# Kernel tuning notes

Measured on AMD Instinct MI355X. Metric: run time of the kernel, lower is better.

The kernel has to match this reference:

```python
import jax, jax.numpy as jnp
import numpy as np

MAXG = 8          # max adaptive sampling grid (boxes generated so ceil(roi_size) <= 8)
SCALE = 0.125     # spatial_scale / ds (ds = 1.0)


def setup_inputs() -> dict:
    key = jax.random.key(0)
    ks = jax.random.split(key, 12)
    bs, N, ch, H, W = 8, 128, 1280, 64, 64
    out_ch, inner = 1024, 5120
    z = jax.random.normal(ks[0], (bs, ch, H, W), jnp.float32)
    # boxes (x1, y1, x2, y2) in 512x512 image coords, sizes in [8, 64] px
    x1 = jax.random.uniform(ks[1], (bs, N), minval=0.0, maxval=448.0)
    y1 = jax.random.uniform(ks[2], (bs, N), minval=0.0, maxval=448.0)
    bw = jax.random.uniform(ks[3], (bs, N), minval=8.0, maxval=64.0)
    bh = jax.random.uniform(ks[4], (bs, N), minval=8.0, maxval=64.0)
    bboxes = jnp.stack([x1, y1, x1 + bw, y1 + bh], axis=-1)

    def lin(k, fan_in, shape):
        return jax.random.normal(k, shape, jnp.float32) * (1.0 / np.sqrt(fan_in))

    W1 = lin(ks[5], ch, (ch, inner)); b1 = jnp.zeros((inner,), jnp.float32)
    W2 = lin(ks[6], inner, (inner, out_ch)); b2 = jnp.zeros((out_ch,), jnp.float32)
    S1 = lin(ks[7], 2, (2, 64)); sb1 = jnp.zeros((64,), jnp.float32)
    S2 = lin(ks[8], 64, (64, 256)); sb2 = jnp.zeros((256,), jnp.float32)
    S3 = lin(ks[9], 256, (256, out_ch)); sb3 = jnp.zeros((out_ch,), jnp.float32)
    O = lin(ks[10], 2 * out_ch, (2 * out_ch, out_ch)); ob = jnp.zeros((out_ch,), jnp.float32)
    return dict(z=z, bboxes=bboxes, W1=W1, b1=b1, W2=W2, b2=b2,
                S1=S1, sb1=sb1, S2=S2, sb2=sb2, S3=S3, sb3=sb3, O=O, ob=ob)


def _prep(c, size):
    # torchvision bilinear border handling for one coordinate axis
    oob = (c < -1.0) | (c > size)
    cc = jnp.clip(c, 0.0, None)
    lo0 = jnp.floor(cc)
    hi_case = lo0 >= size - 1
    lo = jnp.minimum(lo0, size - 1).astype(jnp.int32)
    hi = jnp.minimum(lo0 + 1, size - 1).astype(jnp.int32)
    frac = jnp.where(hi_case, 0.0, cc - lo0)
    return lo, hi, frac, oob


def _roi_align_1x1(z, bboxes):
    # torchvision roi_align, output_size=1, aligned=True, sampling_ratio=-1
    bs, ch, H, W = z.shape
    N = bboxes.shape[1]
    boxes = jax.lax.stop_gradient(bboxes).reshape(-1, 4) * SCALE - 0.5  # aligned
    bidx = jnp.repeat(jnp.arange(bs), N)
    rw = boxes[:, 2] - boxes[:, 0]
    rh = boxes[:, 3] - boxes[:, 1]
    gw = jnp.clip(jnp.ceil(rw), 1, MAXG)   # adaptive grid: ceil(roi_size / 1)
    gh = jnp.clip(jnp.ceil(rh), 1, MAXG)
    count = gh * gw
    i = jnp.arange(MAXG, dtype=jnp.float32)
    ys = boxes[:, 1:2] + (i[None] + 0.5) * rh[:, None] / gh[:, None]  # [R, G]
    xs = boxes[:, 0:1] + (i[None] + 0.5) * rw[:, None] / gw[:, None]
    vy = i[None] < gh[:, None]
    vx = i[None] < gw[:, None]
    yl, yh, fy, oy = _prep(ys, H)
    xl, xh, fx, ox = _prep(xs, W)
    my = (vy & ~oy).astype(z.dtype)
    mx = (vx & ~ox).astype(z.dtype)
    mask = my[:, :, None] * mx[:, None, :]             # [R, G, G]
    hy, ly = 1.0 - fy, fy
    hx, lx = 1.0 - fx, fx
    zt = jnp.transpose(z, (0, 2, 3, 1))                # [bs, H, W, ch]
    acc = jnp.zeros((bs * N, ch), z.dtype)
    corners = [(yl, xl, hy, hx), (yl, xh, hy, lx), (yh, xl, ly, hx), (yh, xh, ly, lx)]
    for yi, xi, wy, wx in corners:
        wt = mask * (wy[:, :, None] * wx[:, None, :])  # [R, G, G]
        v = zt[bidx[:, None, None], yi[:, :, None], xi[:, None, :]]  # [R, G, G, ch]
        acc = acc + jnp.einsum('rgh,rghc->rc', wt, v)
    return (acc / count[:, None]).reshape(bs, N, ch)


def reference(z, bboxes, W1, b1, W2, b2, S1, sb1, S2, sb2, S3, sb3, O, ob):
    x = _roi_align_1x1(z, bboxes)                      # [bs, N, ch]
    x = jax.nn.relu(x @ W1 + b1) @ W2 + b2             # out MLP
    # BBoxSizeEmbedder: (h, w) = (y2 - y1, x2 - x1)
    sz = jnp.stack([bboxes[..., 3] - bboxes[..., 1],
                    bboxes[..., 2] - bboxes[..., 0]], axis=-1)
    e = jax.nn.relu(sz @ S1 + sb1)
    e = jax.nn.relu(e @ S2 + sb2)
    e = e @ S3 + sb3
    return jnp.concatenate([x, e], axis=-1) @ O + ob   # out2
```

## Files before the change

kernel.cpp:

```cpp
#include <hip/hip_runtime.h>

static constexpr int kBS    = 8;
static constexpr int kNROI  = 128;
static constexpr int kR     = kBS * kNROI;
static constexpr int kCH    = 1280;
static constexpr int kH     = 64;
static constexpr int kW     = 64;
static constexpr int kPIX   = kH * kW;
static constexpr int kINNER = 5120;
static constexpr int kOUTC  = 1024;
static constexpr int kXE    = 2 * kOUTC;
static constexpr int kE2    = 256;

typedef _Float16 half8 __attribute__((ext_vector_type(8)));
typedef float floatx4 __attribute__((ext_vector_type(4)));

__device__ __forceinline__ void gload_lds16(const _Float16* g, _Float16* l) {
    __builtin_amdgcn_global_load_lds(
        (const __attribute__((address_space(1))) void*)g,
        (__attribute__((address_space(3))) void*)l,
        16, 0, 0);
}

static constexpr int kPrepConvEnd = 13824;
static constexpr int kPrepMlpEnd  = 14080;
static constexpr int kPrepAllEnd  = 14080 + (kPIX / 64) * (kCH / 64) * kBS;

__global__ __launch_bounds__(256) void prep_all(const float* __restrict__ z,
                                                _Float16* __restrict__ zt,
                                                const float* __restrict__ W1,
                                                const float* __restrict__ W2,
                                                const float* __restrict__ O,
                                                const float* __restrict__ S3,
                                                _Float16* __restrict__ W1t,
                                                _Float16* __restrict__ W2t,
                                                _Float16* __restrict__ Ot,
                                                _Float16* __restrict__ S3t,
                                                const float* __restrict__ bboxes,
                                                const float* __restrict__ S1,
                                                const float* __restrict__ sb1,
                                                const float* __restrict__ S2,
                                                const float* __restrict__ sb2,
                                                _Float16* __restrict__ h2f) {
    __shared__ float smem[64 * 65];
    const int bid = blockIdx.x;
    const int t   = threadIdx.x;

    if (bid < kPrepConvEnd) {
        const float* W; _Float16* Wt; int K, N, tile;
        if (bid < 6400)        { W = W1; Wt = W1t; K = kCH;    N = kINNER; tile = bid; }
        else if (bid < 11520)  { W = W2; Wt = W2t; K = kINNER; N = kOUTC;  tile = bid - 6400; }
        else if (bid < 13568)  { W = O;  Wt = Ot;  K = kXE;    N = kOUTC;  tile = bid - 11520; }
        else                   { W = S3; Wt = S3t; K = kE2;    N = kOUTC;  tile = bid - 13568; }
        const int nt = N / 32;
        const int n0 = (tile % nt) * 32;
        const int k0 = (tile / nt) * 32;
        {
            const int row = t >> 3;
            const int c4  = (t & 7) * 4;
            const float4 v = *(const float4*)&W[(size_t)(k0 + row) * N + n0 + c4];
            float* tl = smem + row * 33 + c4;
            tl[0] = v.x; tl[1] = v.y; tl[2] = v.z; tl[3] = v.w;
        }
        __syncthreads();
        {
            const int n  = t >> 3;
            const int k4 = (t & 7) * 4;
            union { _Float16 h[4]; uint2 u; } pk;
#pragma unroll
            for (int j = 0; j < 4; ++j) pk.h[j] = (_Float16)smem[(k4 + j) * 33 + n];
            *(uint2*)&Wt[(size_t)(n0 + n) * K + k0 + k4] = pk.u;
        }
    } else if (bid < kPrepMlpEnd) {
        const int r0 = (bid - kPrepConvEnd) * 4;
        float* sz = smem;
        float* h1 = smem + 8;
        if (t < 8) {
            const int row = t >> 1;
            const int c   = t & 1;
            const float* bb = bboxes + (size_t)(r0 + row) * 4;
            sz[row * 2 + c] = (c == 0) ? (bb[3] - bb[1]) : (bb[2] - bb[0]);
        }
        __syncthreads();
        {
            const int row = t >> 6;
            const int j   = t & 63;
            const float v = sz[row * 2] * S1[j] + sz[row * 2 + 1] * S1[64 + j] + sb1[j];
            h1[row * 64 + j] = fmaxf(v, 0.0f);
        }
        __syncthreads();
        {
            float acc[4];
            const float b = sb2[t];
#pragma unroll
            for (int row = 0; row < 4; ++row) acc[row] = b;
#pragma unroll 16
            for (int k = 0; k < 64; ++k) {
                const float w = S2[k * 256 + t];
#pragma unroll
                for (int row = 0; row < 4; ++row) acc[row] += h1[row * 64 + k] * w;
            }
#pragma unroll
            for (int row = 0; row < 4; ++row)
                h2f[(size_t)(r0 + row) * kE2 + t] = (_Float16)fmaxf(acc[row], 0.0f);
        }
    } else {
        const int tb   = bid - kPrepMlpEnd;
        const int perB = (kPIX / 64) * (kCH / 64);
        const int b    = tb / perB;
        const int rem  = tb - b * perB;
        const int p0 = (rem % (kPIX / 64)) * 64;
        const int c0 = (rem / (kPIX / 64)) * 64;
        const float* zb = z + (size_t)b * kCH * kPIX;
        _Float16* ztb = zt + (size_t)b * kPIX * kCH;
#pragma unroll
        for (int i = 0; i < 4; ++i) {
            const int idx = t + i * 256;
            const int row = idx >> 4;
            const int c4  = (idx & 15) * 4;
            const float4 v = *(const float4*)&zb[(size_t)(c0 + row) * kPIX + p0 + c4];
            float* tl = smem + row * 65 + c4;
            tl[0] = v.x; tl[1] = v.y; tl[2] = v.z; tl[3] = v.w;
        }
        __syncthreads();
#pragma unroll
        for (int i = 0; i < 4; ++i) {
            const int p  = (t >> 4) + i * 16;
            const int c4 = (t & 15) * 4;
            union { _Float16 h[4]; uint2 u; } pk;
#pragma unroll
            for (int j = 0; j < 4; ++j) pk.h[j] = (_Float16)smem[(c4 + j) * 65 + p];
            *(uint2*)(ztb + (size_t)(p0 + p) * kCH + c0 + c4) = pk.u;
        }
    }
}

struct RoiW {
    int   ymin, xmin, nyd, nxd;
    float ywt[12], xwt[12];
    float invCount;
};

__device__ inline void build_wcons(const float* __restrict__ bboxes, int r, RoiW* L) {
    const float x1 = bboxes[r * 4 + 0] * 0.125f - 0.5f;
    const float y1 = bboxes[r * 4 + 1] * 0.125f - 0.5f;
    const float x2 = bboxes[r * 4 + 2] * 0.125f - 0.5f;
    const float y2 = bboxes[r * 4 + 3] * 0.125f - 0.5f;
    const float rw = x2 - x1, rh = y2 - y1;
    const float gwf = fminf(fmaxf(ceilf(rw), 1.0f), 8.0f);
    const float ghf = fminf(fmaxf(ceilf(rh), 1.0f), 8.0f);
    const int gw = (int)gwf, gh = (int)ghf;
    L->invCount = 1.0f / (gwf * ghf);

#pragma unroll
    for (int i = 0; i < 12; ++i) { L->ywt[i] = 0.0f; L->xwt[i] = 0.0f; }

    int ymin = 0, last = 0;
    for (int g = 0; g < gh; ++g) {
        const float c   = y1 + ((float)g + 0.5f) * rh / ghf;
        const bool oob  = (c < -1.0f) || (c > 64.0f);
        const float cc  = fmaxf(c, 0.0f);
        const float lo0 = floorf(cc);
        const bool hic  = (lo0 >= 63.0f);
        const int lo    = (int)fminf(lo0, 63.0f);
        const int hi    = (int)fminf(lo0 + 1.0f, 63.0f);
        const float fr  = hic ? 0.0f : (cc - lo0);
        const float m   = oob ? 0.0f : 1.0f;
        if (g == 0) ymin = lo;
        const int il = min(lo - ymin, 11);
        const int ih = min(hi - ymin, 11);
        L->ywt[il] += m * (1.0f - fr);
        L->ywt[ih] += m * fr;
        last = hi;
    }
    L->ymin = ymin;
    L->nyd  = min(last - ymin + 1, 12);

    int xmin = 0; last = 0;
    for (int g = 0; g < gw; ++g) {
        const float c   = x1 + ((float)g + 0.5f) * rw / gwf;
        const bool oob  = (c < -1.0f) || (c > 64.0f);
        const float cc  = fmaxf(c, 0.0f);
        const float lo0 = floorf(cc);
        const bool hic  = (lo0 >= 63.0f);
        const int lo    = (int)fminf(lo0, 63.0f);
        const int hi    = (int)fminf(lo0 + 1.0f, 63.0f);
        const float fr  = hic ? 0.0f : (cc - lo0);
        const float m   = oob ? 0.0f : 1.0f;
        if (g == 0) xmin = lo;
        const int il = min(lo - xmin, 11);
        const int ih = min(hi - xmin, 11);
        L->xwt[il] += m * (1.0f - fr);
        L->xwt[ih] += m * fr;
        last = hi;
    }
    L->xmin = xmin;
    L->nxd  = min(last - xmin + 1, 12);
}

__global__ __launch_bounds__(256) void roi_gather_f16_v3(const _Float16* __restrict__ zt,
                                                         const float* __restrict__ bboxes,
                                                         _Float16* __restrict__ x) {
    const int r  = blockIdx.y;
    const int b  = r >> 7;
    const int cg = blockIdx.x * 32;
    const int t  = threadIdx.x;
    __shared__ RoiW L;
    __shared__ int   off[144];
    __shared__ float wt[144];
    __shared__ float accs[8][32][9];
    if (t == 0) build_wcons(bboxes, r, &L);
    __syncthreads();
    const int np = L.nyd * L.nxd;
    if (t < np) {
        const int iy = t / L.nxd;
        const int ix = t - iy * L.nxd;
        off[t] = ((L.ymin + iy) * kW + (L.xmin + ix)) * kCH;
        wt[t]  = L.ywt[iy] * L.xwt[ix];
    }
    __syncthreads();
    const int lc = t & 31;
    const int pg = t >> 5;
    const _Float16* base = zt + (size_t)b * kPIX * kCH + (size_t)(cg + lc) * 8;
    float a[8] = {0.f, 0.f, 0.f, 0.f, 0.f, 0.f, 0.f, 0.f};
    for (int p = pg; p < np; p += 8) {
        const float w = wt[p];
        const half8 v = *(const half8*)(base + off[p]);
#pragma unroll
        for (int q = 0; q < 8; ++q) a[q] += w * (float)v[q];
    }
#pragma unroll
    for (int q = 0; q < 8; ++q) accs[pg][lc][q] = a[q];
    __syncthreads();
    const int rc = t >> 3, ch = t & 7;
    float s = 0.f;
#pragma unroll
    for (int g = 0; g < 8; ++g) s += accs[g][rc][ch];
    x[(size_t)r * kCH + (size_t)(cg + rc) * 8 + ch] = (_Float16)(s * L.invCount);
}

__global__ __launch_bounds__(256) void roi_gather_direct(const float* __restrict__ z,
                                                         const float* __restrict__ bboxes,
                                                         _Float16* __restrict__ x) {
    const int r = blockIdx.x;
    const int b = r >> 7;
    __shared__ RoiW L;
    if (threadIdx.x == 0) build_wcons(bboxes, r, &L);
    __syncthreads();
    const float ic = L.invCount;
    const float* zb = z + (size_t)b * kCH * kPIX;
    for (int c = threadIdx.x; c < kCH; c += 256) {
        const float* zc = zb + (size_t)c * kPIX;
        float acc = 0.f;
        for (int iy = 0; iy < L.nyd; ++iy) {
            const float wy = L.ywt[iy];
            const int base = (L.ymin + iy) * kW + L.xmin;
            for (int ix = 0; ix < L.nxd; ++ix)
                acc += wy * L.xwt[ix] * zc[base + ix];
        }
        x[(size_t)r * kCH + c] = (_Float16)(acc * ic);
    }
}

template <int NSPLIT>
__global__ __launch_bounds__(256) void gemm_f16_sk(const _Float16* __restrict__ A,
                                                   const _Float16* __restrict__ Bt,
                                                   float* __restrict__ P,
                                                   int Kfull) {
    __shared__ _Float16 As[2][128 * 32];
    __shared__ _Float16 Bs[2][128 * 32];
    const int t    = threadIdx.x;
    const int lane = t & 63;
    const int wave = t >> 6;
    const int m0 = blockIdx.y * 128, n0 = blockIdx.x * 128;
    const int Ksplit = Kfull / NSPLIT;
    const int s  = blockIdx.z;
    const int Nn = gridDim.x * 128;
    const int Mm = gridDim.y * 128;

    const int c0 = t, c1 = t + 256;
    const _Float16* Ag0 = A + (size_t)(m0 + (c0 >> 2)) * Kfull + (c0 & 3) * 8 + s * Ksplit;
    const _Float16* Ag1 = A + (size_t)(m0 + (c1 >> 2)) * Kfull + (c1 & 3) * 8 + s * Ksplit;
    const _Float16* Bg0 = Bt + (size_t)(n0 + (c0 >> 2)) * Kfull + (c0 & 3) * 8 + s * Ksplit;
    const _Float16* Bg1 = Bt + (size_t)(n0 + (c1 >> 2)) * Kfull + (c1 & 3) * 8 + s * Ksplit;

    const int wm = (wave >> 1) * 64;
    const int wn = (wave & 1) * 64;
    const int fm = lane & 15;
    const int kq = (lane >> 4) * 8;

    floatx4 acc[4][4];
#pragma unroll
    for (int i = 0; i < 4; ++i)
#pragma unroll
        for (int j = 0; j < 4; ++j) acc[i][j] = (floatx4){0.f, 0.f, 0.f, 0.f};

    const int nsteps = Ksplit / 32;
    gload_lds16(Ag0, &As[0][c0 * 8]);
    gload_lds16(Ag1, &As[0][c1 * 8]);
    gload_lds16(Bg0, &Bs[0][c0 * 8]);
    gload_lds16(Bg1, &Bs[0][c1 * 8]);
    __syncthreads();

    for (int ks = 0; ks < nsteps; ++ks) {
        const int cur = ks & 1;
        if (ks + 1 < nsteps) {
            const int kn = (ks + 1) * 32;
            gload_lds16(Ag0 + kn, &As[cur ^ 1][c0 * 8]);
            gload_lds16(Ag1 + kn, &As[cur ^ 1][c1 * 8]);
            gload_lds16(Bg0 + kn, &Bs[cur ^ 1][c0 * 8]);
            gload_lds16(Bg1 + kn, &Bs[cur ^ 1][c1 * 8]);
        }
        half8 af[4], bfv[4];
#pragma unroll
        for (int i = 0; i < 4; ++i)
            af[i] = *(const half8*)&As[cur][(wm + i * 16 + fm) * 32 + kq];
#pragma unroll
        for (int j = 0; j < 4; ++j)
            bfv[j] = *(const half8*)&Bs[cur][(wn + j * 16 + fm) * 32 + kq];
#pragma unroll
        for (int i = 0; i < 4; ++i)
#pragma unroll
            for (int j = 0; j < 4; ++j)
                acc[i][j] = __builtin_amdgcn_mfma_f32_16x16x32_f16(af[i], bfv[j], acc[i][j], 0, 0, 0);
        __syncthreads();
    }

    float* Pp = P + (size_t)s * Mm * Nn;
    const int qr = (lane >> 4) * 4;
#pragma unroll
    for (int j = 0; j < 4; ++j) {
        const int col = n0 + wn + j * 16 + fm;
#pragma unroll
        for (int i = 0; i < 4; ++i) {
            const int row = m0 + wm + i * 16 + qr;
#pragma unroll
            for (int rr = 0; rr < 4; ++rr)
                Pp[(size_t)(row + rr) * Nn + col] = acc[i][j][rr];
        }
    }
}

__global__ __launch_bounds__(256) void gemm_dual(const _Float16* __restrict__ h2f,
                                                 const _Float16* __restrict__ S3t,
                                                 const float* __restrict__ sb3,
                                                 _Float16* __restrict__ xeR,
                                                 const _Float16* __restrict__ x,
                                                 const _Float16* __restrict__ W1t,
                                                 const float* __restrict__ b1,
                                                 _Float16* __restrict__ h) {
    __shared__ _Float16 As[2][128 * 32];
    __shared__ _Float16 Bs[2][128 * 32];
    const int bid = blockIdx.x;
    const _Float16* A; const _Float16* Bt; const float* bias; _Float16* Out;
    int Kfull, ldc, nbn, tile; bool relu;
    if (bid < 64) {
        A = h2f; Bt = S3t; bias = sb3; Out = xeR;
        Kfull = kE2; ldc = kXE; relu = false; nbn = kOUTC / 128; tile = bid;
    } else {
        A = x; Bt = W1t; bias = b1; Out = h;
        Kfull = kCH; ldc = kINNER; relu = true; nbn = kINNER / 128; tile = bid - 64;
    }
    const int n0 = (tile % nbn) * 128;
    const int m0 = (tile / nbn) * 128;

    const int t    = threadIdx.x;
    const int lane = t & 63;
    const int wave = t >> 6;

    const int c0 = t, c1 = t + 256;
    const _Float16* Ag0 = A + (size_t)(m0 + (c0 >> 2)) * Kfull + (c0 & 3) * 8;
    const _Float16* Ag1 = A + (size_t)(m0 + (c1 >> 2)) * Kfull + (c1 & 3) * 8;
    const _Float16* Bg0 = Bt + (size_t)(n0 + (c0 >> 2)) * Kfull + (c0 & 3) * 8;
    const _Float16* Bg1 = Bt + (size_t)(n0 + (c1 >> 2)) * Kfull + (c1 & 3) * 8;

    const int wm = (wave >> 1) * 64;
    const int wn = (wave & 1) * 64;
    const int fm = lane & 15;
    const int kq = (lane >> 4) * 8;

    floatx4 acc[4][4];
#pragma unroll
    for (int i = 0; i < 4; ++i)
#pragma unroll
        for (int j = 0; j < 4; ++j) acc[i][j] = (floatx4){0.f, 0.f, 0.f, 0.f};

    const int nsteps = Kfull / 32;
    gload_lds16(Ag0, &As[0][c0 * 8]);
    gload_lds16(Ag1, &As[0][c1 * 8]);
    gload_lds16(Bg0, &Bs[0][c0 * 8]);
    gload_lds16(Bg1, &Bs[0][c1 * 8]);
    __syncthreads();

    for (int ks = 0; ks < nsteps; ++ks) {
        const int cur = ks & 1;
        if (ks + 1 < nsteps) {
            const int kn = (ks + 1) * 32;
            gload_lds16(Ag0 + kn, &As[cur ^ 1][c0 * 8]);
            gload_lds16(Ag1 + kn, &As[cur ^ 1][c1 * 8]);
            gload_lds16(Bg0 + kn, &Bs[cur ^ 1][c0 * 8]);
            gload_lds16(Bg1 + kn, &Bs[cur ^ 1][c1 * 8]);
        }
        half8 af[4], bfv[4];
#pragma unroll
        for (int i = 0; i < 4; ++i)
            af[i] = *(const half8*)&As[cur][(wm + i * 16 + fm) * 32 + kq];
#pragma unroll
        for (int j = 0; j < 4; ++j)
            bfv[j] = *(const half8*)&Bs[cur][(wn + j * 16 + fm) * 32 + kq];
#pragma unroll
        for (int i = 0; i < 4; ++i)
#pragma unroll
            for (int j = 0; j < 4; ++j)
                acc[i][j] = __builtin_amdgcn_mfma_f32_16x16x32_f16(af[i], bfv[j], acc[i][j], 0, 0, 0);
        __syncthreads();
    }

    const int qr = (lane >> 4) * 4;
#pragma unroll
    for (int j = 0; j < 4; ++j) {
        const int col = n0 + wn + j * 16 + fm;
        const float bv = bias[col];
#pragma unroll
        for (int i = 0; i < 4; ++i) {
            const int row = m0 + wm + i * 16 + qr;
#pragma unroll
            for (int rr = 0; rr < 4; ++rr) {
                float v = acc[i][j][rr] + bv;
                if (relu) v = fmaxf(v, 0.f);
                Out[(size_t)(row + rr) * ldc + col] = (_Float16)v;
            }
        }
    }
}

template <bool RELU, bool F16OUT, int NSPLIT>
__global__ __launch_bounds__(256) void reduce_splitk(const float* __restrict__ P,
                                                     const float* __restrict__ bias,
                                                     void* __restrict__ Cout,
                                                     int Nn, int ldc) {
    const size_t idx = ((size_t)blockIdx.x * 256 + threadIdx.x) * 4;
    const size_t MN  = (size_t)gridDim.x * 1024;
    const int m = (int)(idx / (size_t)Nn);
    const int n = (int)(idx % (size_t)Nn);
    float4 acc = *(const float4*)(P + idx);
#pragma unroll
    for (int s = 1; s < NSPLIT; ++s) {
        const float4 v = *(const float4*)(P + (size_t)s * MN + idx);
        acc.x += v.x; acc.y += v.y; acc.z += v.z; acc.w += v.w;
    }
    const float4 b4 = *(const float4*)(bias + n);
    acc.x += b4.x; acc.y += b4.y; acc.z += b4.z; acc.w += b4.w;
    if (RELU) {
        acc.x = fmaxf(acc.x, 0.f); acc.y = fmaxf(acc.y, 0.f);
        acc.z = fmaxf(acc.z, 0.f); acc.w = fmaxf(acc.w, 0.f);
    }
    if (F16OUT) {
        union { _Float16 h[4]; uint2 u; } pk;
        pk.h[0] = (_Float16)acc.x; pk.h[1] = (_Float16)acc.y;
        pk.h[2] = (_Float16)acc.z; pk.h[3] = (_Float16)acc.w;
        *(uint2*)((_Float16*)Cout + (size_t)m * ldc + n) = pk.u;
    } else {
        *(float4*)((float*)Cout + (size_t)m * ldc + n) = acc;
    }
}

extern "C" void kernel_launch(void* const* d_in, const int* in_sizes, int n_in,
                              void* d_out, int out_size, void* d_ws, size_t ws_size,
                              hipStream_t stream) {
    (void)in_sizes; (void)n_in; (void)out_size;
    const float* z   = (const float*)d_in[0];
    const float* bb  = (const float*)d_in[1];
    const float* W1  = (const float*)d_in[2];
    const float* b1  = (const float*)d_in[3];
    const float* W2  = (const float*)d_in[4];
    const float* b2  = (const float*)d_in[5];
    const float* S1  = (const float*)d_in[6];
    const float* sb1 = (const float*)d_in[7];
    const float* S2  = (const float*)d_in[8];
    const float* sb2 = (const float*)d_in[9];
    const float* S3  = (const float*)d_in[10];
    const float* sb3 = (const float*)d_in[11];
    const float* O   = (const float*)d_in[12];
    const float* ob  = (const float*)d_in[13];
    float* out = (float*)d_out;

    char* ws = (char*)d_ws;
    size_t off = 0;
    auto alloc = [&](size_t bytes) {
        void* p = ws + off;
        off += (bytes + 255) & ~(size_t)255;
        return p;
    };
    _Float16* x    = (_Float16*)alloc((size_t)kR * kCH * 2);
    _Float16* h    = (_Float16*)alloc((size_t)kR * kINNER * 2);
    _Float16* xe   = (_Float16*)alloc((size_t)kR * kXE * 2);
    _Float16* W1t  = (_Float16*)alloc((size_t)kINNER * kCH * 2);
    _Float16* W2t  = (_Float16*)alloc((size_t)kOUTC * kINNER * 2);
    _Float16* Ot   = (_Float16*)alloc((size_t)kOUTC * kXE * 2);
    _Float16* S3t  = (_Float16*)alloc((size_t)kOUTC * kE2 * 2);
    _Float16* h2f  = (_Float16*)alloc((size_t)kR * kE2 * 2);
    float*    P    = (float*)alloc((size_t)8 * kR * kOUTC * 4);
    const size_t ztBytes = (size_t)kBS * kPIX * kCH * 2;
    _Float16* zt  = (_Float16*)(ws + off);
    const bool useT = (off + ztBytes) <= ws_size;

    hipLaunchKernelGGL(prep_all, dim3(useT ? kPrepAllEnd : kPrepMlpEnd), dim3(256), 0,
                       stream, z, zt, W1, W2, O, S3, W1t, W2t, Ot, S3t,
                       bb, S1, sb1, S2, sb2, h2f);

    if (useT) {
        hipLaunchKernelGGL(roi_gather_f16_v3, dim3(kCH / 256, kR), dim3(256), 0, stream,
                           zt, bb, x);
    } else {
        hipLaunchKernelGGL(roi_gather_direct, dim3(kR), dim3(256), 0, stream, z, bb, x);
    }

    hipLaunchKernelGGL(gemm_dual, dim3(64 + (kINNER / 128) * (kR / 128)), dim3(256), 0,
                       stream, h2f, S3t, sb3, xe + kOUTC, x, W1t, b1, h);

    hipLaunchKernelGGL((gemm_f16_sk<8>), dim3(kOUTC / 128, kR / 128, 8), dim3(256), 0,
                       stream, h, W2t, P, kINNER);
    hipLaunchKernelGGL((reduce_splitk<false, true, 8>),
                       dim3((size_t)kR * kOUTC / 1024), dim3(256), 0, stream,
                       P, b2, xe, kOUTC, kXE);

    hipLaunchKernelGGL((gemm_f16_sk<8>), dim3(kOUTC / 128, kR / 128, 8), dim3(256), 0,
                       stream, xe, Ot, P, kXE);
    hipLaunchKernelGGL((reduce_splitk<false, false, 8>),
                       dim3((size_t)kR * kOUTC / 1024), dim3(256), 0, stream,
                       P, ob, out, kOUTC, kOUTC);
}
```

Before: 419.6 us.

## Replace z transpose and ROI gather with per-plane LDS gather using precomputed sample lists

Removes the full fp32-to-fp16 transpose of z into an NHWC buffer. Instead, the prep kernel precomputes each ROI's list of (pixel offset, weight) pairs with the count division folded into the weight. A new gather kernel loads 4 channel planes of z into LDS and walks those lists for all 128 ROIs of an image. This reads z exactly once at fp32 and skips writing and re-reading the transposed copy, at the cost of low per-block parallelism and serial, per-thread list walks that read pixels from LDS.

```diff
diff --git a/kernel.cpp b/kernel.cpp
--- a/kernel.cpp
+++ b/kernel.cpp
@@ -11,6 +11,7 @@
 static constexpr int kOUTC  = 1024;
 static constexpr int kXE    = 2 * kOUTC;
 static constexpr int kE2    = 256;
+static constexpr int kLB    = 144;
 
 typedef _Float16 half8 __attribute__((ext_vector_type(8)));
 typedef float floatx4 __attribute__((ext_vector_type(4)));
@@ -20,119 +21,6 @@
         (const __attribute__((address_space(1))) void*)g,
         (__attribute__((address_space(3))) void*)l,
         16, 0, 0);
-}
-
-static constexpr int kPrepConvEnd = 13824;
-static constexpr int kPrepMlpEnd  = 14080;
-static constexpr int kPrepAllEnd  = 14080 + (kPIX / 64) * (kCH / 64) * kBS;
-
-__global__ __launch_bounds__(256) void prep_all(const float* __restrict__ z,
-                                                _Float16* __restrict__ zt,
-                                                const float* __restrict__ W1,
-                                                const float* __restrict__ W2,
-                                                const float* __restrict__ O,
-                                                const float* __restrict__ S3,
-                                                _Float16* __restrict__ W1t,
-                                                _Float16* __restrict__ W2t,
-                                                _Float16* __restrict__ Ot,
-                                                _Float16* __restrict__ S3t,
-                                                const float* __restrict__ bboxes,
-                                                const float* __restrict__ S1,
-                                                const float* __restrict__ sb1,
-                                                const float* __restrict__ S2,
-                                                const float* __restrict__ sb2,
-                                                _Float16* __restrict__ h2f) {
-    __shared__ float smem[64 * 65];
-    const int bid = blockIdx.x;
-    const int t   = threadIdx.x;
-
-    if (bid < kPrepConvEnd) {
-        const float* W; _Float16* Wt; int K, N, tile;
-        if (bid < 6400)        { W = W1; Wt = W1t; K = kCH;    N = kINNER; tile = bid; }
-        else if (bid < 11520)  { W = W2; Wt = W2t; K = kINNER; N = kOUTC;  tile = bid - 6400; }
-        else if (bid < 13568)  { W = O;  Wt = Ot;  K = kXE;    N = kOUTC;  tile = bid - 11520; }
-        else                   { W = S3; Wt = S3t; K = kE2;    N = kOUTC;  tile = bid - 13568; }
-        const int nt = N / 32;
-        const int n0 = (tile % nt) * 32;
-        const int k0 = (tile / nt) * 32;
-        {
-            const int row = t >> 3;
-            const int c4  = (t & 7) * 4;
-            const float4 v = *(const float4*)&W[(size_t)(k0 + row) * N + n0 + c4];
-            float* tl = smem + row * 33 + c4;
-            tl[0] = v.x; tl[1] = v.y; tl[2] = v.z; tl[3] = v.w;
-        }
-        __syncthreads();
-        {
-            const int n  = t >> 3;
-            const int k4 = (t & 7) * 4;
-            union { _Float16 h[4]; uint2 u; } pk;
-#pragma unroll
-            for (int j = 0; j < 4; ++j) pk.h[j] = (_Float16)smem[(k4 + j) * 33 + n];
-            *(uint2*)&Wt[(size_t)(n0 + n) * K + k0 + k4] = pk.u;
-        }
-    } else if (bid < kPrepMlpEnd) {
-        const int r0 = (bid - kPrepConvEnd) * 4;
-        float* sz = smem;
-        float* h1 = smem + 8;
-        if (t < 8) {
-            const int row = t >> 1;
-            const int c   = t & 1;
-            const float* bb = bboxes + (size_t)(r0 + row) * 4;
-            sz[row * 2 + c] = (c == 0) ? (bb[3] - bb[1]) : (bb[2] - bb[0]);
-        }
-        __syncthreads();
-        {
-            const int row = t >> 6;
-            const int j   = t & 63;
-            const float v = sz[row * 2] * S1[j] + sz[row * 2 + 1] * S1[64 + j] + sb1[j];
-            h1[row * 64 + j] = fmaxf(v, 0.0f);
-        }
-        __syncthreads();
-        {
-            float acc[4];
-            const float b = sb2[t];
-#pragma unroll
-            for (int row = 0; row < 4; ++row) acc[row] = b;
-#pragma unroll 16
-            for (int k = 0; k < 64; ++k) {
-                const float w = S2[k * 256 + t];
-#pragma unroll
-                for (int row = 0; row < 4; ++row) acc[row] += h1[row * 64 + k] * w;
-            }
-#pragma unroll
-            for (int row = 0; row < 4; ++row)
-                h2f[(size_t)(r0 + row) * kE2 + t] = (_Float16)fmaxf(acc[row], 0.0f);
-        }
-    } else {
-        const int tb   = bid - kPrepMlpEnd;
-        const int perB = (kPIX / 64) * (kCH / 64);
-        const int b    = tb / perB;
-        const int rem  = tb - b * perB;
-        const int p0 = (rem % (kPIX / 64)) * 64;
-        const int c0 = (rem / (kPIX / 64)) * 64;
-        const float* zb = z + (size_t)b * kCH * kPIX;
-        _Float16* ztb = zt + (size_t)b * kPIX * kCH;
-#pragma unroll
-        for (int i = 0; i < 4; ++i) {
-            const int idx = t + i * 256;
-            const int row = idx >> 4;
-            const int c4  = (idx & 15) * 4;
-            const float4 v = *(const float4*)&zb[(size_t)(c0 + row) * kPIX + p0 + c4];
-            float* tl = smem + row * 65 + c4;
-            tl[0] = v.x; tl[1] = v.y; tl[2] = v.z; tl[3] = v.w;
-        }
-        __syncthreads();
-#pragma unroll
-        for (int i = 0; i < 4; ++i) {
-            const int p  = (t >> 4) + i * 16;
-            const int c4 = (t & 15) * 4;
-            union { _Float16 h[4]; uint2 u; } pk;
-#pragma unroll
-            for (int j = 0; j < 4; ++j) pk.h[j] = (_Float16)smem[(c4 + j) * 65 + p];
-            *(uint2*)(ztb + (size_t)(p0 + p) * kCH + c0 + c4) = pk.u;
-        }
-    }
 }
 
 struct RoiW {
@@ -198,67 +86,145 @@
     L->nxd  = min(last - xmin + 1, 12);
 }
 
-__global__ __launch_bounds__(256) void roi_gather_f16_v3(const _Float16* __restrict__ zt,
-                                                         const float* __restrict__ bboxes,
+static constexpr int kPrepConvEnd = 13824;
+static constexpr int kPrepMlpEnd  = 14080;
+static constexpr int kPrepAllEnd  = 14084;
+
+__global__ __launch_bounds__(256) void prep_all(const float* __restrict__ W1,
+                                                const float* __restrict__ W2,
+                                                const float* __restrict__ O,
+                                                const float* __restrict__ S3,
+                                                _Float16* __restrict__ W1t,
+                                                _Float16* __restrict__ W2t,
+                                                _Float16* __restrict__ Ot,
+                                                _Float16* __restrict__ S3t,
+                                                const float* __restrict__ bboxes,
+                                                const float* __restrict__ S1,
+                                                const float* __restrict__ sb1,
+                                                const float* __restrict__ S2,
+                                                const float* __restrict__ sb2,
+                                                _Float16* __restrict__ h2f,
+                                                int2* __restrict__ lst,
+                                                int* __restrict__ npA) {
+    __shared__ float smem[32 * 33];
+    const int bid = blockIdx.x;
+    const int t   = threadIdx.x;
+
+    if (bid < kPrepConvEnd) {
+        const float* W; _Float16* Wt; int K, N, tile;
+        if (bid < 6400)        { W = W1; Wt = W1t; K = kCH;    N = kINNER; tile = bid; }
+        else if (bid < 11520)  { W = W2; Wt = W2t; K = kINNER; N = kOUTC;  tile = bid - 6400; }
+        else if (bid < 13568)  { W = O;  Wt = Ot;  K = kXE;    N = kOUTC;  tile = bid - 11520; }
+        else                   { W = S3; Wt = S3t; K = kE2;    N = kOUTC;  tile = bid - 13568; }
+        const int nt = N / 32;
+        const int n0 = (tile % nt) * 32;
+        const int k0 = (tile / nt) * 32;
+        {
+            const int row = t >> 3;
+            const int c4  = (t & 7) * 4;
+            const float4 v = *(const float4*)&W[(size_t)(k0 + row) * N + n0 + c4];
+            float* tl = smem + row * 33 + c4;
+            tl[0] = v.x; tl[1] = v.y; tl[2] = v.z; tl[3] = v.w;
+        }
+        __syncthreads();
+        {
+            const int n  = t >> 3;
+            const int k4 = (t & 7) * 4;
+            union { _Float16 h[4]; uint2 u; } pk;
+#pragma unroll
+            for (int j = 0; j < 4; ++j) pk.h[j] = (_Float16)smem[(k4 + j) * 33 + n];
+            *(uint2*)&Wt[(size_t)(n0 + n) * K + k0 + k4] = pk.u;
+        }
+    } else if (bid < kPrepMlpEnd) {
+        const int r0 = (bid - kPrepConvEnd) * 4;
+        float* sz = smem;
+        float* h1 = smem + 8;
+        if (t < 8) {
+            const int row = t >> 1;
+            const int c   = t & 1;
+            const float* bb = bboxes + (size_t)(r0 + row) * 4;
+            sz[row * 2 + c] = (c == 0) ? (bb[3] - bb[1]) : (bb[2] - bb[0]);
+        }
+        __syncthreads();
+        {
+            const int row = t >> 6;
+            const int j   = t & 63;
+            const float v = sz[row * 2] * S1[j] + sz[row * 2 + 1] * S1[64 + j] + sb1[j];
+            h1[row * 64 + j] = fmaxf(v, 0.0f);
+        }
+        __syncthreads();
+        {
+            float acc[4];
+            const float b = sb2[t];
+#pragma unroll
+            for (int row = 0; row < 4; ++row) acc[row] = b;
+#pragma unroll 16
+            for (int k = 0; k < 64; ++k) {
+                const float w = S2[k * 256 + t];
+#pragma unroll
+                for (int row = 0; row < 4; ++row) acc[row] += h1[row * 64 + k] * w;
+            }
+#pragma unroll
+            for (int row = 0; row < 4; ++row)
+                h2f[(size_t)(r0 + row) * kE2 + t] = (_Float16)fmaxf(acc[row], 0.0f);
+        }
+    } else {
+        const int r = (bid - kPrepMlpEnd) * 256 + t;
+        RoiW L;
+        build_wcons(bboxes, r, &L);
+        int2* lr = lst + (size_t)r * kLB;
+        int p = 0;
+        for (int iy = 0; iy < L.nyd; ++iy) {
+            const float wy = L.ywt[iy] * L.invCount;
+            const int yb   = (L.ymin + iy) * kW + L.xmin;
+            for (int ix = 0; ix < L.nxd; ++ix) {
+                const float w = wy * L.xwt[ix];
+                if (w != 0.0f) {
+                    int2 e; e.x = yb + ix; e.y = __float_as_int(w);
+                    lr[p++] = e;
+                }
+            }
+        }
+        npA[r] = p;
+    }
+}
+
+static constexpr int kPC = 4;
+static constexpr int kPS = 4112;
+
+__global__ __launch_bounds__(256) void roi_gather_planes(const float* __restrict__ z,
+                                                         const int2* __restrict__ lst,
+                                                         const int* __restrict__ npA,
                                                          _Float16* __restrict__ x) {
-    const int r  = blockIdx.y;
-    const int b  = r >> 7;
-    const int cg = blockIdx.x * 32;
-    const int t  = threadIdx.x;
-    __shared__ RoiW L;
-    __shared__ int   off[144];
-    __shared__ float wt[144];
-    __shared__ float accs[8][32][9];
-    if (t == 0) build_wcons(bboxes, r, &L);
+    __shared__ float pl[kPC * kPS];
+    const int chg = blockIdx.x;
+    const int b   = blockIdx.y;
+    const int c0  = chg * kPC;
+    const int t   = threadIdx.x;
+    const float* zb = z + ((size_t)b * kCH + c0) * kPIX;
+#pragma unroll
+    for (int i = 0; i < 16; ++i) {
+        const int idx = t + i * 256;
+        const int ch  = idx >> 10;
+        const int w4  = (idx & 1023) * 4;
+        const float4 v = *(const float4*)&zb[(size_t)ch * kPIX + w4];
+        *(float4*)&pl[ch * kPS + w4] = v;
+    }
     __syncthreads();
-    const int np = L.nyd * L.nxd;
-    if (t < np) {
-        const int iy = t / L.nxd;
-        const int ix = t - iy * L.nxd;
-        off[t] = ((L.ymin + iy) * kW + (L.xmin + ix)) * kCH;
-        wt[t]  = L.ywt[iy] * L.xwt[ix];
-    }
-    __syncthreads();
-    const int lc = t & 31;
-    const int pg = t >> 5;
-    const _Float16* base = zt + (size_t)b * kPIX * kCH + (size_t)(cg + lc) * 8;
-    float a[8] = {0.f, 0.f, 0.f, 0.f, 0.f, 0.f, 0.f, 0.f};
-    for (int p = pg; p < np; p += 8) {
-        const float w = wt[p];
-        const half8 v = *(const half8*)(base + off[p]);
-#pragma unroll
-        for (int q = 0; q < 8; ++q) a[q] += w * (float)v[q];
-    }
-#pragma unroll
-    for (int q = 0; q < 8; ++q) accs[pg][lc][q] = a[q];
-    __syncthreads();
-    const int rc = t >> 3, ch = t & 7;
-    float s = 0.f;
-#pragma unroll
-    for (int g = 0; g < 8; ++g) s += accs[g][rc][ch];
-    x[(size_t)r * kCH + (size_t)(cg + rc) * 8 + ch] = (_Float16)(s * L.invCount);
-}
-
-__global__ __launch_bounds__(256) void roi_gather_direct(const float* __restrict__ z,
-                                                         const float* __restrict__ bboxes,
-                                                         _Float16* __restrict__ x) {
-    const int r = blockIdx.x;
-    const int b = r >> 7;
-    __shared__ RoiW L;
-    if (threadIdx.x == 0) build_wcons(bboxes, r, &L);
-    __syncthreads();
-    const float ic = L.invCount;
-    const float* zb = z + (size_t)b * kCH * kPIX;
-    for (int c = threadIdx.x; c < kCH; c += 256) {
-        const float* zc = zb + (size_t)c * kPIX;
-        float acc = 0.f;
-        for (int iy = 0; iy < L.nyd; ++iy) {
-            const float wy = L.ywt[iy];
-            const int base = (L.ymin + iy) * kW + L.xmin;
-            for (int ix = 0; ix < L.nxd; ++ix)
-                acc += wy * L.xwt[ix] * zc[base + ix];
-        }
-        x[(size_t)r * kCH + c] = (_Float16)(acc * ic);
+    const int ch   = t & 3;
+    const int slot = t >> 2;
+    const float* plc = pl + ch * kPS;
+#pragma unroll
+    for (int rr = 0; rr < 2; ++rr) {
+        const int r = b * kNROI + slot + rr * 64;
+        const int np = npA[r];
+        const int2* lr = lst + (size_t)r * kLB;
+        float acc = 0.0f;
+        for (int p = 0; p < np; ++p) {
+            const int2 e = lr[p];
+            acc += __int_as_float(e.y) * plc[e.x];
+        }
+        x[(size_t)r * kCH + c0 + ch] = (_Float16)acc;
     }
 }
 
@@ -468,7 +434,7 @@
 extern "C" void kernel_launch(void* const* d_in, const int* in_sizes, int n_in,
                               void* d_out, int out_size, void* d_ws, size_t ws_size,
                               hipStream_t stream) {
-    (void)in_sizes; (void)n_in; (void)out_size;
+    (void)in_sizes; (void)n_in; (void)out_size; (void)ws_size;
     const float* z   = (const float*)d_in[0];
     const float* bb  = (const float*)d_in[1];
     const float* W1  = (const float*)d_in[2];
@@ -500,21 +466,16 @@
     _Float16* Ot   = (_Float16*)alloc((size_t)kOUTC * kXE * 2);
     _Float16* S3t  = (_Float16*)alloc((size_t)kOUTC * kE2 * 2);
     _Float16* h2f  = (_Float16*)alloc((size_t)kR * kE2 * 2);
+    int2*     lst  = (int2*)alloc((size_t)kR * kLB * 8);
+    int*      npA  = (int*)alloc((size_t)kR * 4);
     float*    P    = (float*)alloc((size_t)8 * kR * kOUTC * 4);
-    const size_t ztBytes = (size_t)kBS * kPIX * kCH * 2;
-    _Float16* zt  = (_Float16*)(ws + off);
-    const bool useT = (off + ztBytes) <= ws_size;
-
-    hipLaunchKernelGGL(prep_all, dim3(useT ? kPrepAllEnd : kPrepMlpEnd), dim3(256), 0,
-                       stream, z, zt, W1, W2, O, S3, W1t, W2t, Ot, S3t,
-                       bb, S1, sb1, S2, sb2, h2f);
-
-    if (useT) {
-        hipLaunchKernelGGL(roi_gather_f16_v3, dim3(kCH / 256, kR), dim3(256), 0, stream,
-                           zt, bb, x);
-    } else {
-        hipLaunchKernelGGL(roi_gather_direct, dim3(kR), dim3(256), 0, stream, z, bb, x);
-    }
+
+    hipLaunchKernelGGL(prep_all, dim3(kPrepAllEnd), dim3(256), 0, stream,
+                       W1, W2, O, S3, W1t, W2t, Ot, S3t,
+                       bb, S1, sb1, S2, sb2, h2f, lst, npA);
+
+    hipLaunchKernelGGL(roi_gather_planes, dim3(kCH / kPC, kBS), dim3(256), 0, stream,
+                       z, lst, npA, x);
 
     hipLaunchKernelGGL(gemm_dual, dim3(64 + (kINNER / 128) * (kR / 128)), dim3(256), 0,
                        stream, h2f, S3t, sb3, xe + kOUTC, x, W1t, b1, h);
```

Result: slower. 437.1 us (+4.2%).
